# Optimization experiments

Hardware: AMD Instinct MI355X
Metric: run time of the kernel (lower is better)

## Reference

```python
import jax, jax.numpy as jnp
import numpy as np

A, H, C, N, M = 256, 1024, 1024, 8192, 4096


def _linear(x, W, b):
    return x @ W.T + b


def _cosine_similarity(key_vec, memory):
    # key_vec: (1, M), memory: (N, M)
    k = key_vec / (jnp.linalg.norm(key_vec, axis=1, keepdims=True) + 1e-16)
    m = memory / (jnp.linalg.norm(memory, axis=1, keepdims=True) + 1e-16)
    sim = m @ k.T  # (N, 1)
    # NOTE: faithful to torch: softmax over dim=1, which has size 1 -> all ones
    return jax.nn.softmax(sim, axis=1)


def _circular_convolution(w, s):
    # torch loops: result[i] = sum_j w[(i - j) % N, 0] * s[j, 0]
    # s is the (1, N) shift matrix, so s.shape[0] == 1 (faithful to the torch loop bounds)
    n = w.shape[0]
    J = s.shape[0]
    idx = (jnp.arange(n)[:, None] - jnp.arange(J)[None, :]) % n  # (n, J)
    return (w[idx, 0] @ s[:, 0])[:, None]  # (n, 1)


def _sharpen(w, gamma):
    w = w ** gamma
    return w / jnp.sum(w, axis=0, keepdims=True)


def _gru_step(x, h, W_ih, W_hh, b_ih, b_hh):
    # single-timestep PyTorch GRU cell math
    gi = x @ W_ih.T + b_ih
    gh = h @ W_hh.T + b_hh
    i_r, i_z, i_n = jnp.split(gi, 3, axis=1)
    h_r, h_z, h_n = jnp.split(gh, 3, axis=1)
    r = jax.nn.sigmoid(i_r + h_r)
    z = jax.nn.sigmoid(i_z + h_z)
    n = jnp.tanh(i_n + r * h_n)
    return (1.0 - z) * n + z * h


def setup_inputs() -> dict:
    key = jax.random.key(0)
    ks = jax.random.split(key, 16)
    s = 0.02
    f32 = jnp.float32
    return {
        'action': jax.random.normal(ks[0], (1, A), f32),
        'hidden_state': jax.random.normal(ks[1], (1, 1, H), f32),
        'prev_read_weight': jax.random.uniform(ks[2], (N, 1), f32) / N,
        'prev_write_weight': jax.random.uniform(ks[3], (N, 1), f32) / N,
        'prev_controller_hidden': jax.random.normal(ks[4], (1, 1, C), f32) * 0.1,
        'memory': jax.random.normal(ks[5], (N, M), f32),
        'W_ih': jax.random.normal(ks[6], (3 * C, A + H), f32) * s,
        'W_hh': jax.random.normal(ks[7], (3 * C, C), f32) * s,
        'b_ih': jnp.zeros((3 * C,), f32),
        'b_hh': jnp.zeros((3 * C,), f32),
        'W_read': jax.random.normal(ks[8], (M, C), f32) * s,
        'b_read': jnp.zeros((M,), f32),
        'W_write': jax.random.normal(ks[9], (M, C), f32) * s,
        'b_write': jnp.zeros((M,), f32),
        'W_add': jax.random.normal(ks[10], (M, C), f32) * s,
        'b_add': jnp.zeros((M,), f32),
        'W_erase': jax.random.normal(ks[11], (M, C), f32) * s,
        'b_erase': jnp.zeros((M,), f32),
        'W_shift': jax.random.normal(ks[12], (N, C), f32) * s,
        'b_shift': jnp.zeros((N,), f32),
        'W_gamma': jax.random.normal(ks[13], (1, C), f32) * s,
        'b_gamma': jnp.zeros((1,), f32),
        'W_gate': jax.random.normal(ks[14], (1, C), f32) * s,
        'b_gate': jnp.zeros((1,), f32),
    }


def reference(action, hidden_state, prev_read_weight, prev_write_weight,
              prev_controller_hidden, memory,
              W_ih, W_hh, b_ih, b_hh,
              W_read, b_read, W_write, b_write,
              W_add, b_add, W_erase, b_erase,
              W_shift, b_shift, W_gamma, b_gamma, W_gate, b_gate):
    x = jnp.concatenate([action.reshape(1, -1), hidden_state[-1]], axis=1)  # (1, A+H)
    h = _gru_step(x, prev_controller_hidden[0], W_ih, W_hh, b_ih, b_hh)     # (1, C)
    controller_out = h
    new_controller_hidden = h[None]  # (1, 1, C)

    read_key = _linear(controller_out, W_read, b_read)    # (1, M)
    write_key = _linear(controller_out, W_write, b_write)  # (1, M)
    read_weight = _cosine_similarity(read_key, memory)     # (N, 1)
    write_weight = _cosine_similarity(write_key, memory)   # (N, 1)

    g = jax.nn.sigmoid(_linear(controller_out, W_gate, b_gate))  # (1, 1)
    read_weight = g * read_weight + (1.0 - g) * prev_read_weight
    write_weight = g * write_weight + (1.0 - g) * prev_write_weight

    shift = jax.nn.softmax(_linear(controller_out, W_shift, b_shift), axis=1)  # (1, N)
    gamma = jax.nn.softplus(_linear(controller_out, W_gamma, b_gamma))         # (1, 1)

    read_weight = _sharpen(_circular_convolution(read_weight, shift), gamma)
    write_weight = _sharpen(_circular_convolution(write_weight, shift), gamma)

    read_vector = read_weight.T @ memory  # (1, M)
    add_vec = _linear(controller_out, W_add, b_add)      # (1, M)
    erase_vec = _linear(controller_out, W_erase, b_erase)  # (1, M)
    # memory write (computed but discarded, exactly as in the torch forward which
    # never stores the updated local `memory` back to self.memory)
    _ = memory * (1.0 - write_weight * erase_vec) + write_weight * add_vec

    return (read_vector, read_weight, write_weight, new_controller_hidden)
```

## Files before the change

kernel.cpp:

```cpp
#include <hip/hip_runtime.h>
#include <math.h>

#define AA 256
#define HH 1024
#define CC 1024
#define NN 8192
#define MM 4096

#define WS_G      0
#define WS_GAMMA  1
#define WS_SR     2
#define WS_SW     3
#define GI_OFF    4
#define GH_OFF    (GI_OFF + 3*CC)
#define TR_OFF    (GH_OFF + 3*CC)
#define TW_OFF    (TR_OFF + NN)
#define P_OFF     (TW_OFF + NN)

__device__ __forceinline__ float wave_reduce(float v) {
    #pragma unroll
    for (int o = 32; o > 0; o >>= 1) v += __shfl_down(v, o);
    return v;
}

__global__ __launch_bounds__(256) void k_gru_gates(
    const float* __restrict__ action, const float* __restrict__ hidden,
    const float* __restrict__ W_ih, const float* __restrict__ W_hh,
    const float* __restrict__ b_ih, const float* __restrict__ b_hh,
    const float* __restrict__ hprev, float* __restrict__ ws)
{
    const int t = threadIdx.x;
    const int wid = t >> 6, lane = t & 63;
    const int row = blockIdx.x * 4 + wid;

    const float4* __restrict__ Wih4 = (const float4*)W_ih + (size_t)row * 320;
    const float4* __restrict__ Whh4 = (const float4*)W_hh + (size_t)row * 256;
    const float4* __restrict__ act4 = (const float4*)action;
    const float4* __restrict__ hid4 = (const float4*)hidden;
    const float4* __restrict__ hp4  = (const float4*)hprev;

    float4 a[5], b[4], xa[5], xb[4];
    #pragma unroll
    for (int j = 0; j < 5; ++j) a[j] = Wih4[lane + 64 * j];
    #pragma unroll
    for (int j = 0; j < 4; ++j) b[j] = Whh4[lane + 64 * j];
    xa[0] = act4[lane];
    #pragma unroll
    for (int j = 1; j < 5; ++j) xa[j] = hid4[lane + 64 * (j - 1)];
    #pragma unroll
    for (int j = 0; j < 4; ++j) xb[j] = hp4[lane + 64 * j];

    float si = 0.0f, sh = 0.0f;
    #pragma unroll
    for (int j = 0; j < 5; ++j)
        si += a[j].x * xa[j].x + a[j].y * xa[j].y + a[j].z * xa[j].z + a[j].w * xa[j].w;
    #pragma unroll
    for (int j = 0; j < 4; ++j)
        sh += b[j].x * xb[j].x + b[j].y * xb[j].y + b[j].z * xb[j].z + b[j].w * xb[j].w;

    si = wave_reduce(si);
    sh = wave_reduce(sh);
    if (lane == 0) {
        ws[GI_OFF + row] = si + b_ih[row];
        ws[GH_OFF + row] = sh + b_hh[row];
    }
}

__global__ __launch_bounds__(1024) void k_gru_combine(
    const float* __restrict__ hprev,
    const float* __restrict__ W_gate, const float* __restrict__ b_gate,
    const float* __restrict__ W_gamma, const float* __restrict__ b_gamma,
    float* __restrict__ ws, float* __restrict__ d_out)
{
    const int c = threadIdx.x;
    if (c == 1) ws[WS_SR] = 0.0f;
    if (c == 2) ws[WS_SW] = 0.0f;
    const float* gi = ws + GI_OFF;
    const float* gh = ws + GH_OFF;
    const float r = 1.0f / (1.0f + expf(-(gi[c] + gh[c])));
    const float z = 1.0f / (1.0f + expf(-(gi[CC + c] + gh[CC + c])));
    const float n = tanhf(gi[2 * CC + c] + r * gh[2 * CC + c]);
    const float h = (1.0f - z) * n + z * hprev[c];
    d_out[MM + 2 * NN + c] = h;

    float vg = h * W_gate[c];
    float vm = h * W_gamma[c];
    vg = wave_reduce(vg);
    vm = wave_reduce(vm);
    __shared__ float rg[16], rm[16];
    const int wid = c >> 6;
    if ((c & 63) == 0) { rg[wid] = vg; rm[wid] = vm; }
    __syncthreads();
    if (c == 0) {
        float sg = 0.0f, sm = 0.0f;
        #pragma unroll
        for (int i = 0; i < 16; ++i) { sg += rg[i]; sm += rm[i]; }
        sg += b_gate[0];
        sm += b_gamma[0];
        ws[WS_G] = 1.0f / (1.0f + expf(-sg));
        ws[WS_GAMMA] = (sm > 20.0f) ? sm : log1pf(expf(sm));
    }
}

__global__ __launch_bounds__(256) void k_readvec(
    const float* __restrict__ memory,
    const float* __restrict__ prev_r, const float* __restrict__ prev_w,
    float* __restrict__ ws)
{
    __shared__ float tch[32];
    const int t = threadIdx.x;
    const int bx = blockIdx.x;
    const int by = blockIdx.y;
    const int row0 = by * 32;

    if (t < 32) {
        const float g = ws[WS_G];
        const float gamma = ws[WS_GAMMA];
        const float tr = powf(g + (1.0f - g) * prev_r[row0 + t], gamma);
        tch[t] = tr;
        if (bx == 0) {
            const float tw = powf(g + (1.0f - g) * prev_w[row0 + t], gamma);
            ws[TR_OFF + row0 + t] = tr;
            ws[TW_OFF + row0 + t] = tw;
            float sr = tr, sw = tw;
            #pragma unroll
            for (int o = 16; o > 0; o >>= 1) {
                sr += __shfl_down(sr, o);
                sw += __shfl_down(sw, o);
            }
            if (t == 0) { atomicAdd(&ws[WS_SR], sr); atomicAdd(&ws[WS_SW], sw); }
        }
    }
    __syncthreads();

    const int c4 = bx * 256 + t;
    const float4* __restrict__ mem4 = (const float4*)memory + (size_t)row0 * 1024 + c4;
    float ax = 0.0f, ay = 0.0f, az = 0.0f, aw = 0.0f;
    #pragma unroll
    for (int grp = 0; grp < 4; ++grp) {
        float4 m[8];
        #pragma unroll
        for (int j = 0; j < 8; ++j)
            m[j] = mem4[(size_t)(grp * 8 + j) * 1024];
        #pragma unroll
        for (int j = 0; j < 8; ++j) {
            const float w = tch[grp * 8 + j];
            ax += w * m[j].x; ay += w * m[j].y; az += w * m[j].z; aw += w * m[j].w;
        }
    }
    float4 acc; acc.x = ax; acc.y = ay; acc.z = az; acc.w = aw;
    ((float4*)(ws + P_OFF))[(size_t)by * 1024 + c4] = acc;
}

__global__ __launch_bounds__(256) void k_finalize(
    const float* __restrict__ ws, float* __restrict__ d_out)
{
    const int t = threadIdx.x, b = blockIdx.x;
    if (b < 16) {
        const int col = b * 256 + t;
        const float* __restrict__ P = ws + P_OFF;
        float s0 = 0.0f, s1 = 0.0f, s2 = 0.0f, s3 = 0.0f;
        #pragma unroll 8
        for (int yb = 0; yb < 256; yb += 4) {
            s0 += P[(size_t)(yb + 0) * 4096 + col];
            s1 += P[(size_t)(yb + 1) * 4096 + col];
            s2 += P[(size_t)(yb + 2) * 4096 + col];
            s3 += P[(size_t)(yb + 3) * 4096 + col];
        }
        d_out[col] = (s0 + s1 + s2 + s3) / ws[WS_SR];
    } else {
        const int idx = (b - 16) * 256 + t;
        d_out[MM + idx] = (idx < NN) ? ws[TR_OFF + idx] / ws[WS_SR]
                                     : ws[TW_OFF + idx - NN] / ws[WS_SW];
    }
}

extern "C" void kernel_launch(void* const* d_in, const int* in_sizes, int n_in,
                              void* d_out, int out_size, void* d_ws, size_t ws_size,
                              hipStream_t stream)
{
    const float* action = (const float*)d_in[0];
    const float* hidden = (const float*)d_in[1];
    const float* prev_r = (const float*)d_in[2];
    const float* prev_w = (const float*)d_in[3];
    const float* hprev  = (const float*)d_in[4];
    const float* memory = (const float*)d_in[5];
    const float* W_ih   = (const float*)d_in[6];
    const float* W_hh   = (const float*)d_in[7];
    const float* b_ih   = (const float*)d_in[8];
    const float* b_hh   = (const float*)d_in[9];
    const float* W_gamma = (const float*)d_in[20];
    const float* b_gamma = (const float*)d_in[21];
    const float* W_gate  = (const float*)d_in[22];
    const float* b_gate  = (const float*)d_in[23];

    float* ws  = (float*)d_ws;
    float* out = (float*)d_out;

    hipLaunchKernelGGL(k_gru_gates, dim3(3 * CC / 4), dim3(256), 0, stream,
                       action, hidden, W_ih, W_hh, b_ih, b_hh, hprev, ws);
    hipLaunchKernelGGL(k_gru_combine, dim3(1), dim3(1024), 0, stream,
                       hprev, W_gate, b_gate, W_gamma, b_gamma, ws, out);
    hipLaunchKernelGGL(k_readvec, dim3(4, 256), dim3(256), 0, stream,
                       memory, prev_r, prev_w, ws);
    hipLaunchKernelGGL(k_finalize, dim3(80), dim3(256), 0, stream,
                       ws, out);
}
```

Before: 317.8 us.

## Fuse GRU combine, read-vector and finalize into one kernel with flag sync

Merges the single-block GRU combine, the memory-weighted read pass and the finalize reduction into one persistent-style launch. A flag published by block (0,0) gates the other blocks, and a completion counter gates 64 extra reducer blocks. Each block prefetches its first memory rows before waiting on the flag, so the load overlaps the GRU combine. The finalize reduction is also restructured to use float4 loads with a shared-memory tree. This removes two launches and their gaps, but relies on spin-waiting across blocks, which can deadlock if the waiting blocks are not co-resident with the blocks they wait on.

```diff
diff --git a/kernel.cpp b/kernel.cpp
--- a/kernel.cpp
+++ b/kernel.cpp
@@ -11,7 +11,9 @@
 #define WS_GAMMA  1
 #define WS_SR     2
 #define WS_SW     3
-#define GI_OFF    4
+#define WS_FLAG   4
+#define WS_CTR    5
+#define GI_OFF    8
 #define GH_OFF    (GI_OFF + 3*CC)
 #define TR_OFF    (GH_OFF + 3*CC)
 #define TW_OFF    (TR_OFF + NN)
@@ -33,6 +35,11 @@
     const int wid = t >> 6, lane = t & 63;
     const int row = blockIdx.x * 4 + wid;
 
+    if (blockIdx.x == 0 && t == 0) {
+        ws[WS_SR] = 0.0f; ws[WS_SW] = 0.0f;
+        ((unsigned*)ws)[WS_FLAG] = 0u; ((unsigned*)ws)[WS_CTR] = 0u;
+    }
+
     const float4* __restrict__ Wih4 = (const float4*)W_ih + (size_t)row * 320;
     const float4* __restrict__ Whh4 = (const float4*)W_hh + (size_t)row * 256;
     const float4* __restrict__ act4 = (const float4*)action;
@@ -66,60 +73,122 @@
     }
 }
 
-__global__ __launch_bounds__(1024) void k_gru_combine(
+__global__ __launch_bounds__(256) void k_main(
+    const float* __restrict__ memory,
+    const float* __restrict__ prev_r, const float* __restrict__ prev_w,
     const float* __restrict__ hprev,
     const float* __restrict__ W_gate, const float* __restrict__ b_gate,
     const float* __restrict__ W_gamma, const float* __restrict__ b_gamma,
     float* __restrict__ ws, float* __restrict__ d_out)
 {
-    const int c = threadIdx.x;
-    if (c == 1) ws[WS_SR] = 0.0f;
-    if (c == 2) ws[WS_SW] = 0.0f;
-    const float* gi = ws + GI_OFF;
-    const float* gh = ws + GH_OFF;
-    const float r = 1.0f / (1.0f + expf(-(gi[c] + gh[c])));
-    const float z = 1.0f / (1.0f + expf(-(gi[CC + c] + gh[CC + c])));
-    const float n = tanhf(gi[2 * CC + c] + r * gh[2 * CC + c]);
-    const float h = (1.0f - z) * n + z * hprev[c];
-    d_out[MM + 2 * NN + c] = h;
-
-    float vg = h * W_gate[c];
-    float vm = h * W_gamma[c];
-    vg = wave_reduce(vg);
-    vm = wave_reduce(vm);
-    __shared__ float rg[16], rm[16];
-    const int wid = c >> 6;
-    if ((c & 63) == 0) { rg[wid] = vg; rm[wid] = vm; }
-    __syncthreads();
-    if (c == 0) {
-        float sg = 0.0f, sm = 0.0f;
-        #pragma unroll
-        for (int i = 0; i < 16; ++i) { sg += rg[i]; sm += rm[i]; }
-        sg += b_gate[0];
-        sm += b_gamma[0];
-        ws[WS_G] = 1.0f / (1.0f + expf(-sg));
-        ws[WS_GAMMA] = (sm > 20.0f) ? sm : log1pf(expf(sm));
-    }
-}
-
-__global__ __launch_bounds__(256) void k_readvec(
-    const float* __restrict__ memory,
-    const float* __restrict__ prev_r, const float* __restrict__ prev_w,
-    float* __restrict__ ws)
-{
+    const int t = threadIdx.x;
+    const int bx = blockIdx.x, by = blockIdx.y;
+    unsigned* wsu = (unsigned*)ws;
+
     __shared__ float tch[32];
-    const int t = threadIdx.x;
-    const int bx = blockIdx.x;
-    const int by = blockIdx.y;
+    __shared__ float rgx[4], rmx[4];
+    __shared__ float4 red[256];
+
+    if (by >= 256) {
+        const int rb = (by - 256) * 4 + bx;
+        if (t == 0) {
+            while (__hip_atomic_load(&wsu[WS_CTR], __ATOMIC_RELAXED,
+                                     __HIP_MEMORY_SCOPE_AGENT) < 1024u)
+                __builtin_amdgcn_s_sleep(2);
+            __threadfence();
+        }
+        __syncthreads();
+
+        const int col = t & 15;
+        const int rg  = t >> 4;
+        const int c4  = rb * 16 + col;
+        const float4* __restrict__ P4 = (const float4*)(ws + P_OFF);
+        float4 s = {0.0f, 0.0f, 0.0f, 0.0f};
+        #pragma unroll
+        for (int k = 0; k < 16; ++k) {
+            float4 v = P4[(size_t)(rg * 16 + k) * 1024 + c4];
+            s.x += v.x; s.y += v.y; s.z += v.z; s.w += v.w;
+        }
+        red[t] = s;
+        __syncthreads();
+        if (t < 16) {
+            float4 a = red[t];
+            #pragma unroll
+            for (int g2 = 1; g2 < 16; ++g2) {
+                float4 v = red[g2 * 16 + t];
+                a.x += v.x; a.y += v.y; a.z += v.z; a.w += v.w;
+            }
+            const float inv = 1.0f / ws[WS_SR];
+            float4 o; o.x = a.x * inv; o.y = a.y * inv; o.z = a.z * inv; o.w = a.w * inv;
+            ((float4*)d_out)[rb * 16 + t] = o;
+        }
+        if (t < 64) {
+            const int idx4 = rb * 64 + t;
+            const float inv = (idx4 < 2048) ? 1.0f / ws[WS_SR] : 1.0f / ws[WS_SW];
+            float4 v = ((const float4*)(ws + TR_OFF))[idx4];
+            float4 o; o.x = v.x * inv; o.y = v.y * inv; o.z = v.z * inv; o.w = v.w * inv;
+            ((float4*)d_out)[1024 + idx4] = o;
+        }
+        return;
+    }
+
     const int row0 = by * 32;
-
+    const int c4   = bx * 256 + t;
+    const float4* __restrict__ mem4 = (const float4*)memory + (size_t)row0 * 1024 + c4;
+
+    float4 m0[8];
+    #pragma unroll
+    for (int j = 0; j < 8; ++j) m0[j] = mem4[(size_t)j * 1024];
+    float pr = 0.0f, pw = 0.0f;
+    if (t < 32) { pr = prev_r[row0 + t]; if (bx == 0) pw = prev_w[row0 + t]; }
+
+    if (bx == 0 && by == 0) {
+        const float* gi = ws + GI_OFF;
+        const float* gh = ws + GH_OFF;
+        float vg = 0.0f, vm = 0.0f;
+        #pragma unroll
+        for (int k = 0; k < 4; ++k) {
+            const int c = t + 256 * k;
+            const float r = 1.0f / (1.0f + expf(-(gi[c] + gh[c])));
+            const float z = 1.0f / (1.0f + expf(-(gi[CC + c] + gh[CC + c])));
+            const float n = tanhf(gi[2 * CC + c] + r * gh[2 * CC + c]);
+            const float h = (1.0f - z) * n + z * hprev[c];
+            d_out[MM + 2 * NN + c] = h;
+            vg += h * W_gate[c];
+            vm += h * W_gamma[c];
+        }
+        vg = wave_reduce(vg);
+        vm = wave_reduce(vm);
+        const int wid = t >> 6;
+        if ((t & 63) == 0) { rgx[wid] = vg; rmx[wid] = vm; }
+        __syncthreads();
+        if (t == 0) {
+            const float sg = rgx[0] + rgx[1] + rgx[2] + rgx[3] + b_gate[0];
+            const float sm = rmx[0] + rmx[1] + rmx[2] + rmx[3] + b_gamma[0];
+            ws[WS_G] = 1.0f / (1.0f + expf(-sg));
+            ws[WS_GAMMA] = (sm > 20.0f) ? sm : log1pf(expf(sm));
+            __threadfence();
+            __hip_atomic_store(&wsu[WS_FLAG], 1u, __ATOMIC_RELEASE,
+                               __HIP_MEMORY_SCOPE_AGENT);
+        }
+        __syncthreads();
+    } else {
+        if (t == 0) {
+            while (__hip_atomic_load(&wsu[WS_FLAG], __ATOMIC_RELAXED,
+                                     __HIP_MEMORY_SCOPE_AGENT) == 0u)
+                __builtin_amdgcn_s_sleep(1);
+            __threadfence();
+        }
+        __syncthreads();
+    }
+
+    const float g = ws[WS_G];
+    const float gamma = ws[WS_GAMMA];
     if (t < 32) {
-        const float g = ws[WS_G];
-        const float gamma = ws[WS_GAMMA];
-        const float tr = powf(g + (1.0f - g) * prev_r[row0 + t], gamma);
+        const float tr = powf(g + (1.0f - g) * pr, gamma);
         tch[t] = tr;
         if (bx == 0) {
-            const float tw = powf(g + (1.0f - g) * prev_w[row0 + t], gamma);
+            const float tw = powf(g + (1.0f - g) * pw, gamma);
             ws[TR_OFF + row0 + t] = tr;
             ws[TW_OFF + row0 + t] = tw;
             float sr = tr, sw = tw;
@@ -133,11 +202,14 @@
     }
     __syncthreads();
 
-    const int c4 = bx * 256 + t;
-    const float4* __restrict__ mem4 = (const float4*)memory + (size_t)row0 * 1024 + c4;
     float ax = 0.0f, ay = 0.0f, az = 0.0f, aw = 0.0f;
     #pragma unroll
-    for (int grp = 0; grp < 4; ++grp) {
+    for (int j = 0; j < 8; ++j) {
+        const float w = tch[j];
+        ax += w * m0[j].x; ay += w * m0[j].y; az += w * m0[j].z; aw += w * m0[j].w;
+    }
+    #pragma unroll
+    for (int grp = 1; grp < 4; ++grp) {
         float4 m[8];
         #pragma unroll
         for (int j = 0; j < 8; ++j)
@@ -150,28 +222,12 @@
     }
     float4 acc; acc.x = ax; acc.y = ay; acc.z = az; acc.w = aw;
     ((float4*)(ws + P_OFF))[(size_t)by * 1024 + c4] = acc;
-}
-
-__global__ __launch_bounds__(256) void k_finalize(
-    const float* __restrict__ ws, float* __restrict__ d_out)
-{
-    const int t = threadIdx.x, b = blockIdx.x;
-    if (b < 16) {
-        const int col = b * 256 + t;
-        const float* __restrict__ P = ws + P_OFF;
-        float s0 = 0.0f, s1 = 0.0f, s2 = 0.0f, s3 = 0.0f;
-        #pragma unroll 8
-        for (int yb = 0; yb < 256; yb += 4) {
-            s0 += P[(size_t)(yb + 0) * 4096 + col];
-            s1 += P[(size_t)(yb + 1) * 4096 + col];
-            s2 += P[(size_t)(yb + 2) * 4096 + col];
-            s3 += P[(size_t)(yb + 3) * 4096 + col];
-        }
-        d_out[col] = (s0 + s1 + s2 + s3) / ws[WS_SR];
-    } else {
-        const int idx = (b - 16) * 256 + t;
-        d_out[MM + idx] = (idx < NN) ? ws[TR_OFF + idx] / ws[WS_SR]
-                                     : ws[TW_OFF + idx - NN] / ws[WS_SW];
+
+    __syncthreads();
+    if (t == 0) {
+        __threadfence();
+        __hip_atomic_fetch_add(&wsu[WS_CTR], 1u, __ATOMIC_RELEASE,
+                               __HIP_MEMORY_SCOPE_AGENT);
     }
 }
 
@@ -199,10 +255,7 @@
 
     hipLaunchKernelGGL(k_gru_gates, dim3(3 * CC / 4), dim3(256), 0, stream,
                        action, hidden, W_ih, W_hh, b_ih, b_hh, hprev, ws);
-    hipLaunchKernelGGL(k_gru_combine, dim3(1), dim3(1024), 0, stream,
-                       hprev, W_gate, b_gate, W_gamma, b_gamma, ws, out);
-    hipLaunchKernelGGL(k_readvec, dim3(4, 256), dim3(256), 0, stream,
-                       memory, prev_r, prev_w, ws);
-    hipLaunchKernelGGL(k_finalize, dim3(80), dim3(256), 0, stream,
-                       ws, out);
-}
+    hipLaunchKernelGGL(k_main, dim3(4, 272), dim3(256), 0, stream,
+                       memory, prev_r, prev_w, hprev,
+                       W_gate, b_gate, W_gamma, b_gamma, ws, out);
+}
```

New measurement: 417.4 us. 31.3% more time.

## Compute normalized weights in GRU combine; nontemporal memory loads; parallel finalize reduction

Applied to the files above, without the earlier changes.

Moves the read/write weight sharpening and normalization into the single-block combine kernel, which reduces the sums in-block instead of using atomics, so the read-vector kernel reads pre-normalized weights. Memory loads in the read-vector kernel now use nontemporal loads to avoid polluting the cache with a streaming 128MB read. The finalize reduction becomes a 64-block float4 tree reduction over the partials instead of 16 blocks each serially summing 256 rows. The cost is more serial work in the one-block combine kernel: 16K pow calls on a single CU.

```diff
diff --git a/kernel.cpp b/kernel.cpp
--- a/kernel.cpp
+++ b/kernel.cpp
@@ -9,13 +9,12 @@
 
 #define WS_G      0
 #define WS_GAMMA  1
-#define WS_SR     2
-#define WS_SW     3
 #define GI_OFF    4
 #define GH_OFF    (GI_OFF + 3*CC)
-#define TR_OFF    (GH_OFF + 3*CC)
-#define TW_OFF    (TR_OFF + NN)
-#define P_OFF     (TW_OFF + NN)
+#define WN_OFF    (GH_OFF + 3*CC)
+#define P_OFF     (WN_OFF + NN)
+
+typedef float nt_f4 __attribute__((ext_vector_type(4)));
 
 __device__ __forceinline__ float wave_reduce(float v) {
     #pragma unroll
@@ -68,13 +67,14 @@
 
 __global__ __launch_bounds__(1024) void k_gru_combine(
     const float* __restrict__ hprev,
+    const float* __restrict__ prev_r, const float* __restrict__ prev_w,
     const float* __restrict__ W_gate, const float* __restrict__ b_gate,
     const float* __restrict__ W_gamma, const float* __restrict__ b_gamma,
     float* __restrict__ ws, float* __restrict__ d_out)
 {
     const int c = threadIdx.x;
-    if (c == 1) ws[WS_SR] = 0.0f;
-    if (c == 2) ws[WS_SW] = 0.0f;
+    __shared__ float rg[16], rm[16], bc[4];
+
     const float* gi = ws + GI_OFF;
     const float* gh = ws + GH_OFF;
     const float r = 1.0f / (1.0f + expf(-(gi[c] + gh[c])));
@@ -83,11 +83,8 @@
     const float h = (1.0f - z) * n + z * hprev[c];
     d_out[MM + 2 * NN + c] = h;
 
-    float vg = h * W_gate[c];
-    float vm = h * W_gamma[c];
-    vg = wave_reduce(vg);
-    vm = wave_reduce(vm);
-    __shared__ float rg[16], rm[16];
+    float vg = wave_reduce(h * W_gate[c]);
+    float vm = wave_reduce(h * W_gamma[c]);
     const int wid = c >> 6;
     if ((c & 63) == 0) { rg[wid] = vg; rm[wid] = vm; }
     __syncthreads();
@@ -97,15 +94,48 @@
         for (int i = 0; i < 16; ++i) { sg += rg[i]; sm += rm[i]; }
         sg += b_gate[0];
         sm += b_gamma[0];
-        ws[WS_G] = 1.0f / (1.0f + expf(-sg));
-        ws[WS_GAMMA] = (sm > 20.0f) ? sm : log1pf(expf(sm));
+        const float g = 1.0f / (1.0f + expf(-sg));
+        const float gamma = (sm > 20.0f) ? sm : log1pf(expf(sm));
+        ws[WS_G] = g; ws[WS_GAMMA] = gamma;
+        bc[0] = g; bc[1] = gamma;
+    }
+    __syncthreads();
+    const float g = bc[0], gamma = bc[1];
+
+    float tr[8], tw[8];
+    float sr = 0.0f, sw = 0.0f;
+    #pragma unroll
+    for (int k = 0; k < 8; ++k) {
+        const int row = c + 1024 * k;
+        tr[k] = powf(g + (1.0f - g) * prev_r[row], gamma);
+        tw[k] = powf(g + (1.0f - g) * prev_w[row], gamma);
+        sr += tr[k]; sw += tw[k];
+    }
+    sr = wave_reduce(sr);
+    sw = wave_reduce(sw);
+    if ((c & 63) == 0) { rg[wid] = sr; rm[wid] = sw; }
+    __syncthreads();
+    if (c == 0) {
+        float a = 0.0f, b = 0.0f;
+        #pragma unroll
+        for (int i = 0; i < 16; ++i) { a += rg[i]; b += rm[i]; }
+        bc[2] = 1.0f / a;
+        bc[3] = 1.0f / b;
+    }
+    __syncthreads();
+    const float isr = bc[2], isw = bc[3];
+    #pragma unroll
+    for (int k = 0; k < 8; ++k) {
+        const int row = c + 1024 * k;
+        const float wr = tr[k] * isr;
+        ws[WN_OFF + row]     = wr;
+        d_out[MM + row]      = wr;
+        d_out[MM + NN + row] = tw[k] * isw;
     }
 }
 
 __global__ __launch_bounds__(256) void k_readvec(
-    const float* __restrict__ memory,
-    const float* __restrict__ prev_r, const float* __restrict__ prev_w,
-    float* __restrict__ ws)
+    const float* __restrict__ memory, float* __restrict__ ws)
 {
     __shared__ float tch[32];
     const int t = threadIdx.x;
@@ -113,35 +143,18 @@
     const int by = blockIdx.y;
     const int row0 = by * 32;
 
-    if (t < 32) {
-        const float g = ws[WS_G];
-        const float gamma = ws[WS_GAMMA];
-        const float tr = powf(g + (1.0f - g) * prev_r[row0 + t], gamma);
-        tch[t] = tr;
-        if (bx == 0) {
-            const float tw = powf(g + (1.0f - g) * prev_w[row0 + t], gamma);
-            ws[TR_OFF + row0 + t] = tr;
-            ws[TW_OFF + row0 + t] = tw;
-            float sr = tr, sw = tw;
-            #pragma unroll
-            for (int o = 16; o > 0; o >>= 1) {
-                sr += __shfl_down(sr, o);
-                sw += __shfl_down(sw, o);
-            }
-            if (t == 0) { atomicAdd(&ws[WS_SR], sr); atomicAdd(&ws[WS_SW], sw); }
-        }
-    }
+    if (t < 32) tch[t] = ws[WN_OFF + row0 + t];
     __syncthreads();
 
     const int c4 = bx * 256 + t;
-    const float4* __restrict__ mem4 = (const float4*)memory + (size_t)row0 * 1024 + c4;
+    const nt_f4* __restrict__ mem4 = (const nt_f4*)memory + (size_t)row0 * 1024 + c4;
     float ax = 0.0f, ay = 0.0f, az = 0.0f, aw = 0.0f;
     #pragma unroll
     for (int grp = 0; grp < 4; ++grp) {
-        float4 m[8];
+        nt_f4 m[8];
         #pragma unroll
         for (int j = 0; j < 8; ++j)
-            m[j] = mem4[(size_t)(grp * 8 + j) * 1024];
+            m[j] = __builtin_nontemporal_load(&mem4[(size_t)(grp * 8 + j) * 1024]);
         #pragma unroll
         for (int j = 0; j < 8; ++j) {
             const float w = tch[grp * 8 + j];
@@ -155,23 +168,28 @@
 __global__ __launch_bounds__(256) void k_finalize(
     const float* __restrict__ ws, float* __restrict__ d_out)
 {
-    const int t = threadIdx.x, b = blockIdx.x;
-    if (b < 16) {
-        const int col = b * 256 + t;
-        const float* __restrict__ P = ws + P_OFF;
-        float s0 = 0.0f, s1 = 0.0f, s2 = 0.0f, s3 = 0.0f;
-        #pragma unroll 8
-        for (int yb = 0; yb < 256; yb += 4) {
-            s0 += P[(size_t)(yb + 0) * 4096 + col];
-            s1 += P[(size_t)(yb + 1) * 4096 + col];
-            s2 += P[(size_t)(yb + 2) * 4096 + col];
-            s3 += P[(size_t)(yb + 3) * 4096 + col];
+    __shared__ float4 red[256];
+    const int t = threadIdx.x, rb = blockIdx.x;
+    const int col = t & 15;
+    const int rg  = t >> 4;
+    const int c4  = rb * 16 + col;
+    const float4* __restrict__ P4 = (const float4*)(ws + P_OFF);
+    float4 s = {0.0f, 0.0f, 0.0f, 0.0f};
+    #pragma unroll
+    for (int k = 0; k < 16; ++k) {
+        float4 v = P4[(size_t)(rg * 16 + k) * 1024 + c4];
+        s.x += v.x; s.y += v.y; s.z += v.z; s.w += v.w;
+    }
+    red[t] = s;
+    __syncthreads();
+    if (t < 16) {
+        float4 a = red[t];
+        #pragma unroll
+        for (int g2 = 1; g2 < 16; ++g2) {
+            float4 v = red[g2 * 16 + t];
+            a.x += v.x; a.y += v.y; a.z += v.z; a.w += v.w;
         }
-        d_out[col] = (s0 + s1 + s2 + s3) / ws[WS_SR];
-    } else {
-        const int idx = (b - 16) * 256 + t;
-        d_out[MM + idx] = (idx < NN) ? ws[TR_OFF + idx] / ws[WS_SR]
-                                     : ws[TW_OFF + idx - NN] / ws[WS_SW];
+        ((float4*)d_out)[rb * 16 + t] = a;
     }
 }
 
@@ -200,9 +218,9 @@
     hipLaunchKernelGGL(k_gru_gates, dim3(3 * CC / 4), dim3(256), 0, stream,
                        action, hidden, W_ih, W_hh, b_ih, b_hh, hprev, ws);
     hipLaunchKernelGGL(k_gru_combine, dim3(1), dim3(1024), 0, stream,
-                       hprev, W_gate, b_gate, W_gamma, b_gamma, ws, out);
+                       hprev, prev_r, prev_w, W_gate, b_gate, W_gamma, b_gamma, ws, out);
     hipLaunchKernelGGL(k_readvec, dim3(4, 256), dim3(256), 0, stream,
-                       memory, prev_r, prev_w, ws);
-    hipLaunchKernelGGL(k_finalize, dim3(80), dim3(256), 0, stream,
+                       memory, ws);
+    hipLaunchKernelGGL(k_finalize, dim3(64), dim3(256), 0, stream,
                        ws, out);
 }
```

Result: no change. 312.8 us (-1.6%).
